# Optimization experiments

Hardware: AMD Instinct MI355X
Metric: run time of the kernel (lower is better)

The kernel has to match this reference:

```python
import jax, jax.numpy as jnp
import numpy as np

NN_SIZE = 16
RADIUS2 = 0.5 * 0.5  # radius^2
EPS = 0.0001


def setup_inputs() -> dict:
    key = jax.random.key(0)
    points = jax.random.normal(key, (4, 8192, 3), dtype=jnp.float32)
    return {"points": points}


def reference(points):
    # points: (B, N, 3)
    B, N, C = points.shape
    # Brute-force KNN (pytorch3d ops.knn_points with K = nn_size + 1, self included)
    sq = jnp.sum(points * points, axis=-1)  # (B, N)
    d2_all = sq[:, :, None] + sq[:, None, :] - 2.0 * jnp.einsum('bnc,bmc->bnm', points, points)  # (B,N,N)
    _, idx = jax.lax.top_k(-d2_all, NN_SIZE + 1)  # smallest distances first, (B,N,K+1)
    knn_idx = idx[:, :, 1:]  # drop self, (B, N, K)
    # Gather neighbor coordinates; detached in the original (.detach())
    knn_points = jax.vmap(lambda p, i: p[i])(points, knn_idx)  # (B, N, K, 3)
    knn_points = jax.lax.stop_gradient(knn_points)
    # Recompute squared distances (as the module does)
    knn_v = knn_points - points[:, :, None, :]  # (B, N, K, 3)
    distance2 = jnp.sum(knn_v * knn_v, axis=-1)  # (B, N, K)
    loss = 1.0 / jnp.sqrt(distance2 + EPS)
    loss = jnp.where(distance2 < RADIUS2, loss, jnp.zeros_like(loss))
    # reduction == 'mean'
    return jnp.mean(loss)
```

## Files before the change

kernel.cpp:

```cpp
#include <hip/hip_runtime.h>

#define NPTS 8192
#define NBATCH 4
#define NTOT (NBATCH * NPTS)
#define NN 16
#define RAD2 0.25f
#define EPSF 1e-4f
#define BIGF 1e30f

#define GC 16
#define GP 18
#define CBS 6144
#define NCELL_TOT (NBATCH * CBS)

#define STHR 256
#define SWV 4
#define PPW 2
#define SNB (NTOT / (SWV * PPW))
#define HCAP 384

#define LOG2C 5.0103f
#define NCLAMP 257

#define WS_COUNTS 0
#define WS_RANGES (WS_COUNTS + NCELL_TOT * 4)
#define WS_CURSOR (WS_RANGES + NCELL_TOT * 8)
#define WS_SORTED (WS_CURSOR + NCELL_TOT * 4)
#define WS_BSUMS  (WS_SORTED + (NTOT + 64) * 16)
#define WS_NEEDED (WS_BSUMS + SNB * 4)

__device__ __forceinline__ int cellc(float v) {
  return min(max((int)floorf((v + 4.0f) * 2.0f), 0), GC - 1);
}

__device__ __forceinline__ float prsqrt(float x) {
  float r = __builtin_amdgcn_rsqf(x);
  r = r * fmaf(-0.5f * x * r, r, 1.5f);
  return r;
}

#define CE(a, b) { const float lo_ = fminf(a, b); const float hi_ = fmaxf(a, b); a = lo_; b = hi_; }


__global__ __launch_bounds__(256)
void hist_kernel(const float* __restrict__ pts, int* __restrict__ counts) {
  const int i = blockIdx.x * 256 + threadIdx.x;
  if (i >= NTOT) return;
  const int b = i >> 13;
  const float x = pts[i * 3 + 0], y = pts[i * 3 + 1], z = pts[i * 3 + 2];
  const int c = b * CBS + ((cellc(z) + 1) * GP + (cellc(y) + 1)) * GP + (cellc(x) + 1);
  atomicAdd(&counts[c], 1);
}

__global__ __launch_bounds__(1024)
void scan_kernel(const int* __restrict__ counts, int2* __restrict__ ranges,
                 int* __restrict__ cursor) {
  __shared__ int wtot[16];
  __shared__ int woff[16];
  const int b = blockIdx.x;
  const int tid = threadIdx.x;
  const int wid = tid >> 6;
  const int lane = tid & 63;
  const int g0 = b * CBS + tid * 6;

  int v[6];
  int lsum = 0;
#pragma unroll
  for (int k = 0; k < 6; ++k) { v[k] = counts[g0 + k]; lsum += v[k]; }

  int x = lsum;
  for (int off = 1; off < 64; off <<= 1) {
    const int t = __shfl_up(x, off, 64);
    if (lane >= off) x += t;
  }
  if (lane == 63) wtot[wid] = x;
  __syncthreads();
  if (wid == 0 && lane < 16) {
    int s = wtot[lane];
    for (int off = 1; off < 16; off <<= 1) {
      const int t = __shfl_up(s, off, 64);
      if (lane >= off) s += t;
    }
    woff[lane] = s - wtot[lane];
  }
  __syncthreads();

  int run = b * NPTS + woff[wid] + (x - lsum);
#pragma unroll
  for (int k = 0; k < 6; ++k) {
    ranges[g0 + k] = make_int2(run, v[k]);
    cursor[g0 + k] = run;
    run += v[k];
  }
}

__global__ __launch_bounds__(256)
void scatter_kernel(const float* __restrict__ pts, int* __restrict__ cursor,
                    float4* __restrict__ sorted) {
  const int i = blockIdx.x * 256 + threadIdx.x;
  if (i >= NTOT) return;
  const int b = i >> 13;
  const float x = pts[i * 3 + 0], y = pts[i * 3 + 1], z = pts[i * 3 + 2];
  const int c = b * CBS + ((cellc(z) + 1) * GP + (cellc(y) + 1)) * GP + (cellc(x) + 1);
  const int pos = atomicAdd(&cursor[c], 1);
  sorted[pos] = make_float4(x, y, z, fmaf(x, x, fmaf(y, y, z * z)));
}


__device__ __forceinline__ int scan1(const float4* __restrict__ sorted,
    const int* rs, const int* re, float rr, int selfp,
    float m2x, float m2y, float m2z, float sp, float* __restrict__ hq, int lane) {
  int hcnt = 0;
  const unsigned long long below = (1ull << lane) - 1ull;
#pragma unroll
  for (int m = 0; m < 9; ++m) {
    const int s = rs[m], e = re[m];
    for (int j0 = s; j0 < e; j0 += 64) {
      const int j = j0 + lane;
      float d2 = BIGF;
      if (j < e) {
        const float4 q = sorted[j];
        d2 = fmaf(q.x, m2x, fmaf(q.y, m2y, fmaf(q.z, m2z, q.w + sp)));
      }
      const bool hit = (d2 < rr) && (j != selfp);
      const unsigned long long bal = __ballot(hit);
      const int pos = hcnt + (int)__popcll(bal & below);
      if (hit && pos < HCAP) hq[pos] = d2;
      hcnt += (int)__popcll(bal);
    }
  }
  return hcnt;
}

__device__ __forceinline__ void scan2(const float4* __restrict__ sorted,
    const int* rs, const int* re, float rr,
    int pA, float m2xA, float m2yA, float m2zA, float spA,
    int pB, float m2xB, float m2yB, float m2zB, float spB,
    float* __restrict__ hqA, float* __restrict__ hqB, int lane,
    int& hcntA, int& hcntB) {
  int hA = 0, hB = 0;
  const unsigned long long below = (1ull << lane) - 1ull;
#pragma unroll
  for (int m = 0; m < 9; ++m) {
    const int s = rs[m], e = re[m];
    for (int j0 = s; j0 < e; j0 += 64) {
      const int j = j0 + lane;
      float d2A = BIGF, d2B = BIGF;
      if (j < e) {
        const float4 q = sorted[j];
        const float qw = q.w;
        d2A = fmaf(q.x, m2xA, fmaf(q.y, m2yA, fmaf(q.z, m2zA, qw + spA)));
        d2B = fmaf(q.x, m2xB, fmaf(q.y, m2yB, fmaf(q.z, m2zB, qw + spB)));
      }
      const bool hitA = (d2A < rr) && (j != pA);
      const unsigned long long balA = __ballot(hitA);
      const int posA = hA + (int)__popcll(balA & below);
      if (hitA && posA < HCAP) hqA[posA] = d2A;
      hA += (int)__popcll(balA);
      const bool hitB = (d2B < rr) && (j != pB);
      const unsigned long long balB = __ballot(hitB);
      const int posB = hB + (int)__popcll(balB & below);
      if (hitB && posB < HCAP) hqB[posB] = d2B;
      hB += (int)__popcll(balB);
    }
  }
  hcntA = hA;
  hcntB = hB;
}

template<int R>
__device__ __forceinline__ float tourney(const float* __restrict__ hq, int hn, int lane) {
  float v[R];
#pragma unroll
  for (int r = 0; r < R; ++r) {
    const int idx = lane + 64 * r;
    v[r] = (idx < hn) ? hq[idx] : BIGF;
  }
  if constexpr (R == 3) { CE(v[0], v[1]); CE(v[1], v[2]); CE(v[0], v[1]); }
  if constexpr (R == 6) {
    CE(v[0], v[1]); CE(v[2], v[3]); CE(v[4], v[5]);
    CE(v[1], v[2]); CE(v[3], v[4]);
    CE(v[0], v[1]); CE(v[2], v[3]); CE(v[4], v[5]);
    CE(v[1], v[2]); CE(v[3], v[4]);
    CE(v[0], v[1]); CE(v[2], v[3]); CE(v[4], v[5]);
    CE(v[1], v[2]); CE(v[3], v[4]);
  }
  float loss = 0.0f;
#pragma unroll
  for (int r = 0; r < NN; ++r) {
    float g = v[0];
    g = fminf(g, __shfl_xor(g, 1));
    g = fminf(g, __shfl_xor(g, 2));
    g = fminf(g, __shfl_xor(g, 4));
    g = fminf(g, __shfl_xor(g, 8));
    g = fminf(g, __shfl_xor(g, 16));
    g = fminf(g, __shfl_xor(g, 32));
    loss += prsqrt(g + EPSF);
    const unsigned long long own = __ballot(v[0] == g);
    const int first = (int)(__ffsll((unsigned long long)own) - 1);
    if (lane == first) {
#pragma unroll
      for (int r2 = 0; r2 < R - 1; ++r2) v[r2] = v[r2 + 1];
      v[R - 1] = BIGF;
    }
  }
  return loss;
}

__device__ __forceinline__ float extract_loss(const float* __restrict__ hq, int hn, int lane) {
  if (hn <= 64) {
    float v = (lane < hn) ? hq[lane] : BIGF;
#pragma unroll
    for (int k = 2; k <= 64; k <<= 1) {
#pragma unroll
      for (int j = k >> 1; j > 0; j >>= 1) {
        const float o = __shfl_xor(v, j, 64);
        const bool keepmin = (((lane & j) == 0) != ((lane & k) != 0));
        v = keepmin ? fminf(v, o) : fmaxf(v, o);
      }
    }
    float l = (lane < NN && v < RAD2) ? prsqrt(v + EPSF) : 0.0f;
    l += __shfl_xor(l, 1);
    l += __shfl_xor(l, 2);
    l += __shfl_xor(l, 4);
    l += __shfl_xor(l, 8);
    l += __shfl_xor(l, 16);
    l += __shfl_xor(l, 32);
    return l;
  } else if (hn <= 192) {
    return tourney<3>(hq, hn, lane);
  }
  return tourney<6>(hq, hn, lane);
}


__global__ __launch_bounds__(STHR)
void search_kernel(const float4* __restrict__ sorted, const int2* __restrict__ rngs,
                   float* __restrict__ bsums) {
  __shared__ float hbuf[SWV][2][HCAP];
  __shared__ float wloss[SWV];

  const int tid = threadIdx.x;
  const int wv = tid >> 6;
  const int lane = tid & 63;
  const int pair = wv * SNB + blockIdx.x;
  const int p0 = pair * 2;
  const int p1 = p0 + 1;
  const int bb = p0 >> 13;

  const float4 ptA = sorted[p0];
  const float4 ptB = sorted[p1];
  const float m2xA = -2.0f * ptA.x, m2yA = -2.0f * ptA.y, m2zA = -2.0f * ptA.z;
  const float spA = ptA.w;
  const float m2xB = -2.0f * ptB.x, m2yB = -2.0f * ptB.y, m2zB = -2.0f * ptB.z;
  const float spB = ptB.w;

  const int rbA = __builtin_amdgcn_readfirstlane(
      bb * CBS + ((cellc(ptA.z) + 1) * GP + (cellc(ptA.y) + 1)) * GP);
  const int rbB = __builtin_amdgcn_readfirstlane(
      bb * CBS + ((cellc(ptB.z) + 1) * GP + (cellc(ptB.y) + 1)) * GP);
  const int xA = __builtin_amdgcn_readfirstlane(cellc(ptA.x));
  const int xB = __builtin_amdgcn_readfirstlane(cellc(ptB.x));

  const int rowoff[9] = {
    (-1 * GP - 1) * GP, (-1 * GP + 0) * GP, (-1 * GP + 1) * GP,
    ( 0 * GP - 1) * GP, ( 0 * GP + 0) * GP, ( 0 * GP + 1) * GP,
    ( 1 * GP - 1) * GP, ( 1 * GP + 0) * GP, ( 1 * GP + 1) * GP };

  float* hqA = hbuf[wv][0];
  float* hqB = hbuf[wv][1];
  int hnA, hnB;

  if (rbA == rbB) {
    const int lo = min(xA, xB);
    const int hi = max(xA, xB) + 2;
    int rs[9], re[9], ncand = 0;
#pragma unroll
    for (int m = 0; m < 9; ++m) {
      const int base = rbA + rowoff[m];
      const int2 a = rngs[base + lo];
      const int2 b = rngs[base + hi];
      rs[m] = a.x;
      re[m] = b.x + b.y;
      ncand += re[m] - rs[m];
    }
    const bool clamped = (ncand <= NCLAMP);
    float r0sq = RAD2;
    if (!clamped) r0sq = exp2f((LOG2C - log2f((float)ncand)) * (2.0f / 3.0f));

    int hA, hB;
    scan2(sorted, rs, re, r0sq, p0, m2xA, m2yA, m2zA, spA,
          p1, m2xB, m2yB, m2zB, spB, hqA, hqB, lane, hA, hB);
    hnA = min(hA, HCAP);
    hnB = min(hB, HCAP);
    if (hnA < NN && !clamped)
      hnA = min(scan1(sorted, rs, re, RAD2, p0, m2xA, m2yA, m2zA, spA, hqA, lane), HCAP);
    if (hnB < NN && !clamped)
      hnB = min(scan1(sorted, rs, re, RAD2, p1, m2xB, m2yB, m2zB, spB, hqB, lane), HCAP);
  } else {
    int rsA[9], reA[9], ncA = 0, rsB[9], reB[9], ncB = 0;
#pragma unroll
    for (int m = 0; m < 9; ++m) {
      const int baseA = rbA + rowoff[m];
      const int2 a0 = rngs[baseA + xA];
      const int2 a1 = rngs[baseA + xA + 2];
      rsA[m] = a0.x; reA[m] = a1.x + a1.y; ncA += reA[m] - rsA[m];
      const int baseB = rbB + rowoff[m];
      const int2 b0 = rngs[baseB + xB];
      const int2 b1 = rngs[baseB + xB + 2];
      rsB[m] = b0.x; reB[m] = b1.x + b1.y; ncB += reB[m] - rsB[m];
    }
    const bool clA = (ncA <= NCLAMP);
    const bool clB = (ncB <= NCLAMP);
    float rA = RAD2, rB = RAD2;
    if (!clA) rA = exp2f((LOG2C - log2f((float)ncA)) * (2.0f / 3.0f));
    if (!clB) rB = exp2f((LOG2C - log2f((float)ncB)) * (2.0f / 3.0f));
    hnA = min(scan1(sorted, rsA, reA, rA, p0, m2xA, m2yA, m2zA, spA, hqA, lane), HCAP);
    if (hnA < NN && !clA)
      hnA = min(scan1(sorted, rsA, reA, RAD2, p0, m2xA, m2yA, m2zA, spA, hqA, lane), HCAP);
    hnB = min(scan1(sorted, rsB, reB, rB, p1, m2xB, m2yB, m2zB, spB, hqB, lane), HCAP);
    if (hnB < NN && !clB)
      hnB = min(scan1(sorted, rsB, reB, RAD2, p1, m2xB, m2yB, m2zB, spB, hqB, lane), HCAP);
  }

  const float lossA = extract_loss(hqA, hnA, lane);
  const float lossB = extract_loss(hqB, hnB, lane);

  if (lane == 0) wloss[wv] = lossA + lossB;
  __syncthreads();
  if (tid == 0) {
    float s = 0.0f;
#pragma unroll
    for (int w = 0; w < SWV; ++w) s += wloss[w];
    bsums[blockIdx.x] = s;
  }
}

__global__ __launch_bounds__(256)
void finalize_kernel(const float* __restrict__ block_sums, int nblocks,
                     float* __restrict__ out) {
  __shared__ float s[256];
  float v = 0.0f;
  for (int idx = threadIdx.x; idx < nblocks; idx += 256) v += block_sums[idx];
  s[threadIdx.x] = v;
  __syncthreads();
  for (int off = 128; off > 0; off >>= 1) {
    if (threadIdx.x < off) s[threadIdx.x] += s[threadIdx.x + off];
    __syncthreads();
  }
  if (threadIdx.x == 0) out[0] = s[0] / (float)(NBATCH * NPTS * NN);
}


#define DTILE 1024
#define DNT 512
#define DNW 8
#define DNB (NTOT / 64)
#define CSTRIDE 17
#define QTRIG 13

__device__ __forceinline__ void insert16(float (&td)[NN], float& thrmax, float v) {
  if (v < thrmax) {
    bool done = false;
#pragma unroll
    for (int k = 0; k < NN; ++k) {
      const bool hit = (!done) && (td[k] == thrmax);
      if (hit) td[k] = v;
      done = done || hit;
    }
    thrmax = td[0];
#pragma unroll
    for (int k = 1; k < NN; ++k) thrmax = fmaxf(thrmax, td[k]);
  }
}

__device__ __forceinline__ void drain_queue(float* buf, int qbase, int& cnt,
                                            float (&td)[NN], float& thrmax) {
#pragma unroll
  for (int c = 0; c < 16; ++c) {
    const float v = (c < cnt) ? buf[qbase + c] : BIGF;
    insert16(td, thrmax, v);
  }
  cnt = 0;
}

__global__ __launch_bounds__(DNT)
void dense_kernel(const float* __restrict__ pts, float* __restrict__ block_sums) {
  __shared__ float4 tile[DTILE];
  __shared__ float buf[DNT * CSTRIDE];

  const int tid = threadIdx.x;
  const int wave = tid >> 6;
  const int lane = tid & 63;
  const int bid = blockIdx.x;
  const int b = bid / (NPTS / 64);
  const int base = (bid % (NPTS / 64)) * 64;
  const float* __restrict__ bp = pts + (size_t)b * NPTS * 3;

  const int i = base + lane;
  const float xi = bp[i * 3 + 0];
  const float yi = bp[i * 3 + 1];
  const float zi = bp[i * 3 + 2];

  float td[NN];
#pragma unroll
  for (int k = 0; k < NN; ++k) td[k] = BIGF;
  float thrmax = BIGF;
  int cnt = 0;
  const int qbase = tid * CSTRIDE;

  for (int tb = 0; tb < NPTS; tb += DTILE) {
    for (int pp = tid; pp < DTILE; pp += DNT) {
      const float* sp = bp + (size_t)(tb + pp) * 3;
      tile[pp] = make_float4(sp[0], sp[1], sp[2], 0.0f);
    }
    __syncthreads();
    const int jb = wave * (DTILE / DNW);
    for (int jj = 0; jj < DTILE / DNW; ++jj) {
      const float4 q = tile[jb + jj];
      const float ddx = q.x - xi, ddy = q.y - yi, ddz = q.z - zi;
      const float d2 = fmaf(ddx, ddx, fmaf(ddy, ddy, ddz * ddz));
      if (d2 < RAD2 && d2 != 0.0f) {
        buf[qbase + cnt] = d2;
        ++cnt;
      }
      if (__any(cnt >= QTRIG)) drain_queue(buf, qbase, cnt, td, thrmax);
    }
    __syncthreads();
  }
  drain_queue(buf, qbase, cnt, td, thrmax);
#pragma unroll
  for (int k = 0; k < NN; ++k) buf[qbase + k] = td[k];
  __syncthreads();

  if (wave == 0) {
    float sd[NN];
#pragma unroll
    for (int k = 0; k < NN; ++k) sd[k] = BIGF;
    float smax = BIGF;
    for (int w = 0; w < DNW; ++w) {
      for (int c = 0; c < NN; ++c) {
        insert16(sd, smax, buf[(w * 64 + lane) * CSTRIDE + c]);
      }
    }
    float loss = 0.0f;
#pragma unroll
    for (int k = 0; k < NN; ++k) {
      if (sd[k] < RAD2) loss += 1.0f / sqrtf(sd[k] + EPSF);
    }
    for (int off = 32; off > 0; off >>= 1) loss += __shfl_down(loss, off);
    if (lane == 0) block_sums[bid] = loss;
  }
}


extern "C" void kernel_launch(void* const* d_in, const int* in_sizes, int n_in,
                              void* d_out, int out_size, void* d_ws, size_t ws_size,
                              hipStream_t stream) {
  const float* pts = (const float*)d_in[0];
  float* out = (float*)d_out;
  char* ws = (char*)d_ws;

  if (ws_size >= (size_t)WS_NEEDED) {
    int* counts = (int*)(ws + WS_COUNTS);
    int2* rngs = (int2*)(ws + WS_RANGES);
    int* cursor = (int*)(ws + WS_CURSOR);
    float4* sorted = (float4*)(ws + WS_SORTED);
    float* bsums = (float*)(ws + WS_BSUMS);

    hipMemsetAsync(counts, 0, NCELL_TOT * 4, stream);
    hist_kernel<<<(NTOT + 255) / 256, 256, 0, stream>>>(pts, counts);
    scan_kernel<<<NBATCH, 1024, 0, stream>>>(counts, rngs, cursor);
    scatter_kernel<<<(NTOT + 255) / 256, 256, 0, stream>>>(pts, cursor, sorted);
    search_kernel<<<SNB, STHR, 0, stream>>>(sorted, rngs, bsums);
    finalize_kernel<<<1, 256, 0, stream>>>(bsums, SNB, out);
  } else {
    float* bsums = (float*)ws;
    dense_kernel<<<DNB, DNT, 0, stream>>>(pts, bsums);
    finalize_kernel<<<1, 256, 0, stream>>>(bsums, DNB, out);
  }
}
```

Before: 60.98 us.

## Use persistent waves with atomic work-stealing over point pairs and fast-path small heaps

The search kernel now launches a fixed grid of persistent blocks in which each wave claims point pairs dynamically through a global atomic counter, instead of one pair per wave in a static grid. This is meant to balance uneven per-pair work caused by varying neighborhood density and to remove the per-block syncthreads reduction. Per-pair losses are written to a larger bsums array that finalize must then reduce, and the counter is zeroed by extending the memset. A fast path in extract_loss skips the bitonic sort when at most NN candidates were found.

```diff
diff --git a/kernel.cpp b/kernel.cpp
--- a/kernel.cpp
+++ b/kernel.cpp
@@ -15,19 +15,21 @@
 
 #define STHR 256
 #define SWV 4
-#define PPW 2
-#define SNB (NTOT / (SWV * PPW))
+#define SGRID 2048
+#define NWAVES (SGRID * SWV)
+#define NPAIRS (NTOT / 2)
 #define HCAP 384
 
 #define LOG2C 5.0103f
 #define NCLAMP 257
 
 #define WS_COUNTS 0
-#define WS_RANGES (WS_COUNTS + NCELL_TOT * 4)
+#define WS_CTR    (WS_COUNTS + NCELL_TOT * 4)
+#define WS_RANGES (WS_CTR + 16)
 #define WS_CURSOR (WS_RANGES + NCELL_TOT * 8)
 #define WS_SORTED (WS_CURSOR + NCELL_TOT * 4)
 #define WS_BSUMS  (WS_SORTED + (NTOT + 64) * 16)
-#define WS_NEEDED (WS_BSUMS + SNB * 4)
+#define WS_NEEDED (WS_BSUMS + NPAIRS * 4)
 
 __device__ __forceinline__ int cellc(float v) {
   return min(max((int)floorf((v + 4.0f) * 2.0f), 0), GC - 1);
@@ -208,6 +210,16 @@
 }
 
 __device__ __forceinline__ float extract_loss(const float* __restrict__ hq, int hn, int lane) {
+  if (hn <= NN) {
+    float l = (lane < hn) ? prsqrt(hq[lane] + EPSF) : 0.0f;
+    l += __shfl_xor(l, 1);
+    l += __shfl_xor(l, 2);
+    l += __shfl_xor(l, 4);
+    l += __shfl_xor(l, 8);
+    l += __shfl_xor(l, 16);
+    l += __shfl_xor(l, 32);
+    return l;
+  }
   if (hn <= 64) {
     float v = (lane < hn) ? hq[lane] : BIGF;
 #pragma unroll
@@ -236,103 +248,103 @@
 
 __global__ __launch_bounds__(STHR)
 void search_kernel(const float4* __restrict__ sorted, const int2* __restrict__ rngs,
-                   float* __restrict__ bsums) {
+                   int* __restrict__ ctr, float* __restrict__ bsums) {
   __shared__ float hbuf[SWV][2][HCAP];
-  __shared__ float wloss[SWV];
 
   const int tid = threadIdx.x;
   const int wv = tid >> 6;
   const int lane = tid & 63;
-  const int pair = wv * SNB + blockIdx.x;
-  const int p0 = pair * 2;
-  const int p1 = p0 + 1;
-  const int bb = p0 >> 13;
-
-  const float4 ptA = sorted[p0];
-  const float4 ptB = sorted[p1];
-  const float m2xA = -2.0f * ptA.x, m2yA = -2.0f * ptA.y, m2zA = -2.0f * ptA.z;
-  const float spA = ptA.w;
-  const float m2xB = -2.0f * ptB.x, m2yB = -2.0f * ptB.y, m2zB = -2.0f * ptB.z;
-  const float spB = ptB.w;
-
-  const int rbA = __builtin_amdgcn_readfirstlane(
-      bb * CBS + ((cellc(ptA.z) + 1) * GP + (cellc(ptA.y) + 1)) * GP);
-  const int rbB = __builtin_amdgcn_readfirstlane(
-      bb * CBS + ((cellc(ptB.z) + 1) * GP + (cellc(ptB.y) + 1)) * GP);
-  const int xA = __builtin_amdgcn_readfirstlane(cellc(ptA.x));
-  const int xB = __builtin_amdgcn_readfirstlane(cellc(ptB.x));
+  float* hqA = hbuf[wv][0];
+  float* hqB = hbuf[wv][1];
 
   const int rowoff[9] = {
     (-1 * GP - 1) * GP, (-1 * GP + 0) * GP, (-1 * GP + 1) * GP,
     ( 0 * GP - 1) * GP, ( 0 * GP + 0) * GP, ( 0 * GP + 1) * GP,
     ( 1 * GP - 1) * GP, ( 1 * GP + 0) * GP, ( 1 * GP + 1) * GP };
 
-  float* hqA = hbuf[wv][0];
-  float* hqB = hbuf[wv][1];
-  int hnA, hnB;
-
-  if (rbA == rbB) {
-    const int lo = min(xA, xB);
-    const int hi = max(xA, xB) + 2;
-    int rs[9], re[9], ncand = 0;
-#pragma unroll
-    for (int m = 0; m < 9; ++m) {
-      const int base = rbA + rowoff[m];
-      const int2 a = rngs[base + lo];
-      const int2 b = rngs[base + hi];
-      rs[m] = a.x;
-      re[m] = b.x + b.y;
-      ncand += re[m] - rs[m];
-    }
-    const bool clamped = (ncand <= NCLAMP);
-    float r0sq = RAD2;
-    if (!clamped) r0sq = exp2f((LOG2C - log2f((float)ncand)) * (2.0f / 3.0f));
-
-    int hA, hB;
-    scan2(sorted, rs, re, r0sq, p0, m2xA, m2yA, m2zA, spA,
-          p1, m2xB, m2yB, m2zB, spB, hqA, hqB, lane, hA, hB);
-    hnA = min(hA, HCAP);
-    hnB = min(hB, HCAP);
-    if (hnA < NN && !clamped)
-      hnA = min(scan1(sorted, rs, re, RAD2, p0, m2xA, m2yA, m2zA, spA, hqA, lane), HCAP);
-    if (hnB < NN && !clamped)
-      hnB = min(scan1(sorted, rs, re, RAD2, p1, m2xB, m2yB, m2zB, spB, hqB, lane), HCAP);
-  } else {
-    int rsA[9], reA[9], ncA = 0, rsB[9], reB[9], ncB = 0;
-#pragma unroll
-    for (int m = 0; m < 9; ++m) {
-      const int baseA = rbA + rowoff[m];
-      const int2 a0 = rngs[baseA + xA];
-      const int2 a1 = rngs[baseA + xA + 2];
-      rsA[m] = a0.x; reA[m] = a1.x + a1.y; ncA += reA[m] - rsA[m];
-      const int baseB = rbB + rowoff[m];
-      const int2 b0 = rngs[baseB + xB];
-      const int2 b1 = rngs[baseB + xB + 2];
-      rsB[m] = b0.x; reB[m] = b1.x + b1.y; ncB += reB[m] - rsB[m];
-    }
-    const bool clA = (ncA <= NCLAMP);
-    const bool clB = (ncB <= NCLAMP);
-    float rA = RAD2, rB = RAD2;
-    if (!clA) rA = exp2f((LOG2C - log2f((float)ncA)) * (2.0f / 3.0f));
-    if (!clB) rB = exp2f((LOG2C - log2f((float)ncB)) * (2.0f / 3.0f));
-    hnA = min(scan1(sorted, rsA, reA, rA, p0, m2xA, m2yA, m2zA, spA, hqA, lane), HCAP);
-    if (hnA < NN && !clA)
-      hnA = min(scan1(sorted, rsA, reA, RAD2, p0, m2xA, m2yA, m2zA, spA, hqA, lane), HCAP);
-    hnB = min(scan1(sorted, rsB, reB, rB, p1, m2xB, m2yB, m2zB, spB, hqB, lane), HCAP);
-    if (hnB < NN && !clB)
-      hnB = min(scan1(sorted, rsB, reB, RAD2, p1, m2xB, m2yB, m2zB, spB, hqB, lane), HCAP);
-  }
-
-  const float lossA = extract_loss(hqA, hnA, lane);
-  const float lossB = extract_loss(hqB, hnB, lane);
-
-  if (lane == 0) wloss[wv] = lossA + lossB;
-  __syncthreads();
-  if (tid == 0) {
-    float s = 0.0f;
-#pragma unroll
-    for (int w = 0; w < SWV; ++w) s += wloss[w];
-    bsums[blockIdx.x] = s;
+  int pair = blockIdx.x * SWV + wv;
+
+  while (pair < NPAIRS) {
+    const int p0 = pair * 2;
+    const int p1 = p0 + 1;
+    const int bb = p0 >> 13;
+
+    const float4 ptA = sorted[p0];
+    const float4 ptB = sorted[p1];
+    const float m2xA = -2.0f * ptA.x, m2yA = -2.0f * ptA.y, m2zA = -2.0f * ptA.z;
+    const float spA = ptA.w;
+    const float m2xB = -2.0f * ptB.x, m2yB = -2.0f * ptB.y, m2zB = -2.0f * ptB.z;
+    const float spB = ptB.w;
+
+    const int rbA = __builtin_amdgcn_readfirstlane(
+        bb * CBS + ((cellc(ptA.z) + 1) * GP + (cellc(ptA.y) + 1)) * GP);
+    const int rbB = __builtin_amdgcn_readfirstlane(
+        bb * CBS + ((cellc(ptB.z) + 1) * GP + (cellc(ptB.y) + 1)) * GP);
+    const int xA = __builtin_amdgcn_readfirstlane(cellc(ptA.x));
+    const int xB = __builtin_amdgcn_readfirstlane(cellc(ptB.x));
+
+    int hnA, hnB;
+
+    if (rbA == rbB) {
+      const int lo = min(xA, xB);
+      const int hi = max(xA, xB) + 2;
+      int rs[9], re[9], ncand = 0;
+#pragma unroll
+      for (int m = 0; m < 9; ++m) {
+        const int base = rbA + rowoff[m];
+        const int2 a = rngs[base + lo];
+        const int2 b = rngs[base + hi];
+        rs[m] = a.x;
+        re[m] = b.x + b.y;
+        ncand += re[m] - rs[m];
+      }
+      const bool clamped = (ncand <= NCLAMP);
+      float r0sq = RAD2;
+      if (!clamped) r0sq = exp2f((LOG2C - log2f((float)ncand)) * (2.0f / 3.0f));
+
+      int hA, hB;
+      scan2(sorted, rs, re, r0sq, p0, m2xA, m2yA, m2zA, spA,
+            p1, m2xB, m2yB, m2zB, spB, hqA, hqB, lane, hA, hB);
+      hnA = min(hA, HCAP);
+      hnB = min(hB, HCAP);
+      if (hnA < NN && !clamped)
+        hnA = min(scan1(sorted, rs, re, RAD2, p0, m2xA, m2yA, m2zA, spA, hqA, lane), HCAP);
+      if (hnB < NN && !clamped)
+        hnB = min(scan1(sorted, rs, re, RAD2, p1, m2xB, m2yB, m2zB, spB, hqB, lane), HCAP);
+    } else {
+      int rsA[9], reA[9], ncA = 0, rsB[9], reB[9], ncB = 0;
+#pragma unroll
+      for (int m = 0; m < 9; ++m) {
+        const int baseA = rbA + rowoff[m];
+        const int2 a0 = rngs[baseA + xA];
+        const int2 a1 = rngs[baseA + xA + 2];
+        rsA[m] = a0.x; reA[m] = a1.x + a1.y; ncA += reA[m] - rsA[m];
+        const int baseB = rbB + rowoff[m];
+        const int2 b0 = rngs[baseB + xB];
+        const int2 b1 = rngs[baseB + xB + 2];
+        rsB[m] = b0.x; reB[m] = b1.x + b1.y; ncB += reB[m] - rsB[m];
+      }
+      const bool clA = (ncA <= NCLAMP);
+      const bool clB = (ncB <= NCLAMP);
+      float rA = RAD2, rB = RAD2;
+      if (!clA) rA = exp2f((LOG2C - log2f((float)ncA)) * (2.0f / 3.0f));
+      if (!clB) rB = exp2f((LOG2C - log2f((float)ncB)) * (2.0f / 3.0f));
+      hnA = min(scan1(sorted, rsA, reA, rA, p0, m2xA, m2yA, m2zA, spA, hqA, lane), HCAP);
+      if (hnA < NN && !clA)
+        hnA = min(scan1(sorted, rsA, reA, RAD2, p0, m2xA, m2yA, m2zA, spA, hqA, lane), HCAP);
+      hnB = min(scan1(sorted, rsB, reB, rB, p1, m2xB, m2yB, m2zB, spB, hqB, lane), HCAP);
+      if (hnB < NN && !clB)
+        hnB = min(scan1(sorted, rsB, reB, RAD2, p1, m2xB, m2yB, m2zB, spB, hqB, lane), HCAP);
+    }
+
+    const float lossA = extract_loss(hqA, hnA, lane);
+    const float lossB = extract_loss(hqB, hnB, lane);
+    if (lane == 0) bsums[pair] = lossA + lossB;
+
+    int nv = 0;
+    if (lane == 0) nv = atomicAdd(ctr, 1);
+    nv = __builtin_amdgcn_readfirstlane(nv);
+    pair = NWAVES + nv;
   }
 }
 
@@ -463,17 +475,18 @@
 
   if (ws_size >= (size_t)WS_NEEDED) {
     int* counts = (int*)(ws + WS_COUNTS);
+    int* ctr = (int*)(ws + WS_CTR);
     int2* rngs = (int2*)(ws + WS_RANGES);
     int* cursor = (int*)(ws + WS_CURSOR);
     float4* sorted = (float4*)(ws + WS_SORTED);
     float* bsums = (float*)(ws + WS_BSUMS);
 
-    hipMemsetAsync(counts, 0, NCELL_TOT * 4, stream);
+    hipMemsetAsync(counts, 0, NCELL_TOT * 4 + 16, stream);
     hist_kernel<<<(NTOT + 255) / 256, 256, 0, stream>>>(pts, counts);
     scan_kernel<<<NBATCH, 1024, 0, stream>>>(counts, rngs, cursor);
     scatter_kernel<<<(NTOT + 255) / 256, 256, 0, stream>>>(pts, cursor, sorted);
-    search_kernel<<<SNB, STHR, 0, stream>>>(sorted, rngs, bsums);
-    finalize_kernel<<<1, 256, 0, stream>>>(bsums, SNB, out);
+    search_kernel<<<SGRID, STHR, 0, stream>>>(sorted, rngs, ctr, bsums);
+    finalize_kernel<<<1, 256, 0, stream>>>(bsums, NPAIRS, out);
   } else {
     float* bsums = (float*)ws;
     dense_kernel<<<DNB, DNT, 0, stream>>>(pts, bsums);
```

Result: slower. 234.0 us (+283.7%).
